# Optimization experiments

Measured on AMD Instinct MI355X. Metric: run time of the kernel, lower is better.

Reference implementation:

```python
import jax, jax.numpy as jnp
import numpy as np

IN_F, OUT_F, RANK = 4096, 4096, 1024
B, S = 4, 2048


def soft_threshold24(w):
    """Soft-threshold 2:4 sparsification along the last dim.
    For each group of 4, the two smallest-magnitude entries are zeroed and the
    kept entries are shrunk by the threshold (2nd-smallest magnitude)."""
    g = w.reshape(-1, 4)
    m = jnp.abs(g)
    t = jnp.sort(m, axis=-1)[:, 1:2]  # largest pruned magnitude per group
    sp = jnp.sign(g) * jnp.maximum(m - t, 0.0)
    return sp.reshape(w.shape)


def fake_fp8_mm(a, b):
    """FP8-simulated GEMM: fp16 operands, fp32 accumulate/output (matches fake_fp8_mm)."""
    return jnp.matmul(a.astype(jnp.float16), b.astype(jnp.float16),
                      preferred_element_type=jnp.float32)


def setup_inputs() -> dict:
    key = jax.random.key(0)
    k1, k2, k3 = jax.random.split(key, 3)
    x = jax.random.normal(k1, (B, S, IN_F), dtype=jnp.float32)
    std_a = (2.0 / (IN_F + RANK)) ** 0.5   # xavier_normal for (in_features, rank)
    std_b = (2.0 / (OUT_F + RANK)) ** 0.5  # xavier_normal for (out_features, rank)
    weight_A = jax.random.normal(k2, (IN_F, RANK), dtype=jnp.float32) * std_a
    weight_B = jax.random.normal(k3, (OUT_F, RANK), dtype=jnp.float32) * std_b
    bias = jnp.zeros((OUT_F,), dtype=jnp.float32)
    scale_A = jnp.ones((), dtype=jnp.float32)  # sparse_init_scale buffer
    scale_B = jnp.ones((), dtype=jnp.float32)
    return {"x": x, "weight_A": weight_A, "weight_B": weight_B, "bias": bias,
            "scale_A": scale_A, "scale_B": scale_B}


def reference(x, weight_A, weight_B, bias, scale_A, scale_B):
    # sparse low-rank factors
    wa = soft_threshold24(weight_A) * scale_A  # (in, rank)
    wb = soft_threshold24(weight_B) * scale_B  # (out, rank)
    lead = x.shape[:-1]
    xf = x.reshape(-1, x.shape[-1])            # (T, in)
    x_proj = fake_fp8_mm(xf, wa)               # (T, rank) == x @ A_sparse
    out = fake_fp8_mm(x_proj, wb.T) + bias     # (T, out) == x_proj @ B_sparse^T + b
    return out.reshape(*lead, OUT_F)
```

## Files before the change

### kernel.cpp

```cpp
#include <hip/hip_runtime.h>

#define IN_FEAT 4096
#define OUT_FEAT 4096
#define RANK 1024
#define TOK 8192

typedef _Float16 f16x8 __attribute__((ext_vector_type(8)));
typedef _Float16 f16x4 __attribute__((ext_vector_type(4)));
typedef float f32x4 __attribute__((ext_vector_type(4)));

#define GLD_LDS16(g, l)                                                         \
  __builtin_amdgcn_global_load_lds(                                             \
      (__attribute__((address_space(1))) const void*)(g),                       \
      (__attribute__((address_space(3))) void*)(l), 16, 0, 0)

#define MIDBAR()                                        \
  __builtin_amdgcn_s_barrier();                         \
  asm volatile("s_waitcnt lgkmcnt(0)" ::: "memory")
#define ENDBAR() __builtin_amdgcn_s_barrier()


__device__ __forceinline__ void soft24(const float4 g, float s,
                                       float& r0, float& r1, float& r2, float& r3) {
  const float m0 = fabsf(g.x), m1 = fabsf(g.y), m2 = fabsf(g.z), m3 = fabsf(g.w);
  const float lo1 = fminf(m0, m1), hi1 = fmaxf(m0, m1);
  const float lo2 = fminf(m2, m3), hi2 = fmaxf(m2, m3);
  const float t = fminf(fmaxf(lo1, lo2), fminf(hi1, hi2));
  r0 = copysignf(fmaxf(m0 - t, 0.0f), g.x) * s;
  r1 = copysignf(fmaxf(m1 - t, 0.0f), g.y) * s;
  r2 = copysignf(fmaxf(m2 - t, 0.0f), g.z) * s;
  r3 = copysignf(fmaxf(m3 - t, 0.0f), g.w) * s;
}

__global__ __launch_bounds__(256) void sparsify_A_kernel(
    const float* __restrict__ wA, const float* __restrict__ scaleA,
    _Float16* __restrict__ waT) {
  const int idx = blockIdx.x * 256 + threadIdx.x;
  const int i = idx & (IN_FEAT - 1);
  const int jg = idx >> 12;
  const float4 g = *reinterpret_cast<const float4*>(wA + (size_t)i * RANK + jg * 4);
  const float s = scaleA[0];
  float r0, r1, r2, r3;
  soft24(g, s, r0, r1, r2, r3);
  const size_t base = (size_t)(jg * 4) * IN_FEAT + i;
  waT[base] = (_Float16)r0;
  waT[base + IN_FEAT] = (_Float16)r1;
  waT[base + 2 * IN_FEAT] = (_Float16)r2;
  waT[base + 3 * IN_FEAT] = (_Float16)r3;
}

__global__ __launch_bounds__(256) void sparsify_B_kernel(
    const float* __restrict__ wB, const float* __restrict__ scaleB,
    _Float16* __restrict__ wbs) {
  const int idx = blockIdx.x * 256 + threadIdx.x;
  const float4 g = *reinterpret_cast<const float4*>(wB + (size_t)idx * 4);
  const float s = scaleB[0];
  float r0, r1, r2, r3;
  soft24(g, s, r0, r1, r2, r3);
  f16x4 h;
  h[0] = (_Float16)r0; h[1] = (_Float16)r1; h[2] = (_Float16)r2; h[3] = (_Float16)r3;
  *reinterpret_cast<f16x4*>(wbs + (size_t)idx * 4) = h;
}

template <int N, int K, bool A_F32, bool OUT_F16>
__global__ __launch_bounds__(256, 4) void gemm128(
    const void* __restrict__ Av, const _Float16* __restrict__ Bh,
    void* __restrict__ Cv, const float* __restrict__ bias) {
  __shared__ __attribute__((aligned(128))) char lds[32768];
  char* ldsA = lds;
  char* ldsB = lds + 16384;

  const int tid = threadIdx.x;
  const int lane = tid & 63;
  const int w = tid >> 6;
  const int wrow = (w >> 1) * 64;
  const int wcol = (w & 1) * 64;

  constexpr int GX = N / 128;
  const int nwg = GX * (TOK / 128);
  const int l = blockIdx.y * GX + blockIdx.x;
  const int wg = (l & 7) * (nwg >> 3) + (l >> 3);
  const int brow = (wg / GX) * 128;
  const int bcol = (wg % GX) * 128;

  f32x4 acc[4][4] = {};

  for (int k0 = 0; k0 < K; k0 += 64) {
    __syncthreads();
#pragma unroll
    for (int it = 0; it < 4; ++it) {
      const int c = it * 256 + tid;
      const int row = c >> 3;
      const int u = c & 7;
      const _Float16* gsrc =
          Bh + (size_t)(bcol + row) * K + k0 + ((u ^ (row & 7)) << 3);
      GLD_LDS16(gsrc, ldsB + c * 16);
    }
    if constexpr (A_F32) {
      const float* Af = (const float*)Av;
#pragma unroll
      for (int it = 0; it < 4; ++it) {
        const int c = it * 256 + tid;
        const int row = c >> 3;
        const int u = c & 7;
        const float* gsrc = Af + (size_t)(brow + row) * K + k0 + (u << 3);
        const float4 f0 = *reinterpret_cast<const float4*>(gsrc);
        const float4 f1 = *reinterpret_cast<const float4*>(gsrc + 4);
        f16x8 h;
        h[0] = (_Float16)f0.x; h[1] = (_Float16)f0.y;
        h[2] = (_Float16)f0.z; h[3] = (_Float16)f0.w;
        h[4] = (_Float16)f1.x; h[5] = (_Float16)f1.y;
        h[6] = (_Float16)f1.z; h[7] = (_Float16)f1.w;
        *reinterpret_cast<f16x8*>(ldsA + row * 128 + ((u ^ (row & 7)) << 4)) = h;
      }
    } else {
      const _Float16* Ah = (const _Float16*)Av;
#pragma unroll
      for (int it = 0; it < 4; ++it) {
        const int c = it * 256 + tid;
        const int row = c >> 3;
        const int u = c & 7;
        const _Float16* gsrc =
            Ah + (size_t)(brow + row) * K + k0 + ((u ^ (row & 7)) << 3);
        GLD_LDS16(gsrc, ldsA + c * 16);
      }
    }
    __syncthreads();
#pragma unroll
    for (int kk = 0; kk < 2; ++kk) {
      f16x8 af[4], bf[4];
#pragma unroll
      for (int m = 0; m < 4; ++m) {
        const int row = wrow + m * 16 + (lane & 15);
        const int u = (kk * 4 + (lane >> 4)) ^ (row & 7);
        af[m] = *reinterpret_cast<const f16x8*>(ldsA + row * 128 + u * 16);
      }
#pragma unroll
      for (int n = 0; n < 4; ++n) {
        const int row = wcol + n * 16 + (lane & 15);
        const int u = (kk * 4 + (lane >> 4)) ^ (row & 7);
        bf[n] = *reinterpret_cast<const f16x8*>(ldsB + row * 128 + u * 16);
      }
#pragma unroll
      for (int m = 0; m < 4; ++m)
#pragma unroll
        for (int n = 0; n < 4; ++n)
          acc[m][n] =
              __builtin_amdgcn_mfma_f32_16x16x32_f16(af[m], bf[n], acc[m][n], 0, 0, 0);
    }
  }

  const int r4 = (lane >> 4) * 4;
  const int cl = lane & 15;
  if constexpr (OUT_F16) {
    _Float16* C = (_Float16*)Cv;
#pragma unroll
    for (int m = 0; m < 4; ++m)
#pragma unroll
      for (int n = 0; n < 4; ++n)
#pragma unroll
        for (int j = 0; j < 4; ++j) {
          const int rr = brow + wrow + m * 16 + r4 + j;
          const int cc = bcol + wcol + n * 16 + cl;
          C[(size_t)rr * N + cc] = (_Float16)acc[m][n][j];
        }
  } else {
    float* C = (float*)Cv;
#pragma unroll
    for (int n = 0; n < 4; ++n) {
      const int cc = bcol + wcol + n * 16 + cl;
      const float bv = bias[cc];
#pragma unroll
      for (int m = 0; m < 4; ++m)
#pragma unroll
        for (int j = 0; j < 4; ++j) {
          const int rr = brow + wrow + m * 16 + r4 + j;
          C[(size_t)rr * N + cc] = acc[m][n][j] + bv;
        }
    }
  }
}

template <int M, int N, int K>
__global__ __launch_bounds__(512, 1) void gemm1_f(
    const float* __restrict__ A, const _Float16* __restrict__ B,
    _Float16* __restrict__ C) {
  extern __shared__ char lds[];

  const int tid = threadIdx.x;
  const int lane = tid & 63;
  const int w = tid >> 6;
  const int wr = w >> 2;
  const int wc = w & 3;
  const int l15 = lane & 15;
  const int ubase = lane >> 4;

  constexpr int GX = N / 256;
  constexpr int NWG = GX * (M / 128);
  const int l = blockIdx.y * GX + blockIdx.x;
  const int wg = (l & 7) * (NWG >> 3) + (l >> 3);
  const int brow = (wg / GX) * 128;
  const int bcol = (wg % GX) * 256;

  f32x4 acc[4][4] = {};
  f16x8 af[4][2], bf[4][2];

  const int ar0 = tid >> 3, au0 = tid & 7;
  const int ar1 = (512 + tid) >> 3, au1 = tid & 7;
  float4 a0l, a0h, a1l, a1h;

  auto issueA = [&](int kof) {
    const float* p0 = A + (size_t)(brow + ar0) * K + kof + au0 * 8;
    const float* p1 = A + (size_t)(brow + ar1) * K + kof + au1 * 8;
    a0l = *reinterpret_cast<const float4*>(p0);
    a0h = *reinterpret_cast<const float4*>(p0 + 4);
    a1l = *reinterpret_cast<const float4*>(p1);
    a1h = *reinterpret_cast<const float4*>(p1 + 4);
  };
  auto writeA = [&](int slot) {
    f16x8 h0, h1;
    h0[0] = (_Float16)a0l.x; h0[1] = (_Float16)a0l.y;
    h0[2] = (_Float16)a0l.z; h0[3] = (_Float16)a0l.w;
    h0[4] = (_Float16)a0h.x; h0[5] = (_Float16)a0h.y;
    h0[6] = (_Float16)a0h.z; h0[7] = (_Float16)a0h.w;
    h1[0] = (_Float16)a1l.x; h1[1] = (_Float16)a1l.y;
    h1[2] = (_Float16)a1l.z; h1[3] = (_Float16)a1l.w;
    h1[4] = (_Float16)a1h.x; h1[5] = (_Float16)a1h.y;
    h1[6] = (_Float16)a1h.z; h1[7] = (_Float16)a1h.w;
    *reinterpret_cast<f16x8*>(lds + slot * 16384 + ar0 * 128 +
                              ((au0 ^ (ar0 & 7)) << 4)) = h0;
    *reinterpret_cast<f16x8*>(lds + slot * 16384 + ar1 * 128 +
                              ((au1 ^ (ar1 & 7)) << 4)) = h1;
  };
  auto stageB = [&](int kof, int slot) {
#pragma unroll
    for (int r = 0; r < 4; ++r) {
      const int c = r * 512 + tid;
      const int row = c >> 3;
      const int u = c & 7;
      GLD_LDS16(B + (size_t)(bcol + row) * K + kof + ((u ^ (row & 7)) << 3),
                lds + 49152 + slot * 32768 + c * 16);
    }
  };

  constexpr int NT = K / 64;

  issueA(0);
  stageB(0, 0);
  asm volatile("s_waitcnt vmcnt(4)" ::: "memory");
  writeA(0);
  issueA(64);
  stageB(64, 1);
  asm volatile("s_waitcnt vmcnt(8)" ::: "memory");
  asm volatile("s_waitcnt lgkmcnt(0)" ::: "memory");
  __builtin_amdgcn_s_barrier();

  int slot = 0;
  for (int t = 0; t < NT; ++t) {
#pragma unroll
    for (int i = 0; i < 4; ++i)
#pragma unroll
      for (int ks = 0; ks < 2; ++ks) {
        const int row = wr * 64 + i * 16 + l15;
        const int u = (ks * 4 + ubase) ^ (row & 7);
        af[i][ks] =
            *reinterpret_cast<const f16x8*>(lds + slot * 16384 + row * 128 + u * 16);
      }
#pragma unroll
    for (int j = 0; j < 4; ++j)
#pragma unroll
      for (int ks = 0; ks < 2; ++ks) {
        const int row = wc * 64 + j * 16 + l15;
        const int u = (ks * 4 + ubase) ^ (row & 7);
        bf[j][ks] = *reinterpret_cast<const f16x8*>(lds + 49152 + slot * 32768 +
                                                    row * 128 + u * 16);
      }
    if (t + 1 < NT) {
      int s1 = slot + 1;
      if (s1 >= 3) s1 -= 3;
      writeA(s1);
    }
    if (t + 2 < NT) {
      int s2 = slot + 2;
      if (s2 >= 3) s2 -= 3;
      issueA((t + 2) * 64);
      stageB((t + 2) * 64, s2);
      asm volatile("s_waitcnt vmcnt(8)" ::: "memory");
    } else {
      asm volatile("s_waitcnt vmcnt(0)" ::: "memory");
    }
    MIDBAR();
    __builtin_amdgcn_s_setprio(1);
#pragma unroll
    for (int ks = 0; ks < 2; ++ks)
#pragma unroll
      for (int i = 0; i < 4; ++i)
#pragma unroll
        for (int j = 0; j < 4; ++j)
          acc[i][j] = __builtin_amdgcn_mfma_f32_16x16x32_f16(
              bf[j][ks], af[i][ks], acc[i][j], 0, 0, 0);
    __builtin_amdgcn_s_setprio(0);
    ENDBAR();
    ++slot;
    if (slot == 3) slot = 0;
  }

  const int r4 = (lane >> 4) * 4;
#pragma unroll
  for (int m = 0; m < 4; ++m)
#pragma unroll
    for (int n = 0; n < 4; ++n) {
      const int rr = brow + wr * 64 + m * 16 + l15;
      const int cc = bcol + wc * 64 + n * 16 + r4;
      f16x4 h;
#pragma unroll
      for (int j = 0; j < 4; ++j) h[j] = (_Float16)acc[m][n][j];
      *reinterpret_cast<f16x4*>(C + (size_t)rr * N + cc) = h;
    }
}

#define AOFF(s, h) (((s) * 2 + (h)) * 16384)
#define BOFF(s, h) (65536 + ((s) * 2 + (h)) * 16384)

template <int M, int N, int K>
__global__ __launch_bounds__(512, 2) void gemm2_m(
    const _Float16* __restrict__ A, const _Float16* __restrict__ B,
    float* __restrict__ C, const float* __restrict__ bias) {
  extern __shared__ char lds[];

  const int tid = threadIdx.x;
  const int lane = tid & 63;
  const int w = tid >> 6;
  const int wr = w >> 2;
  const int wc = w & 3;
  const int l15 = lane & 15;
  const int ubase = lane >> 4;

  constexpr int GX = N / 256;
  constexpr int NWG = GX * (M / 256);
  const int l = blockIdx.y * GX + blockIdx.x;
  const int wg = (l & 7) * (NWG >> 3) + (l >> 3);
  const int brow = (wg / GX) * 256;
  const int bcol = (wg % GX) * 256;

  const _Float16* Abase = A + (size_t)brow * K;
  const _Float16* Bbase = B + (size_t)bcol * K;

  auto stage = [&](const _Float16* srcBase, int rowOff, int kof, int ldsOff) {
#pragma unroll
    for (int r = 0; r < 2; ++r) {
      const int c = r * 512 + tid;
      const int row = c >> 3;
      const int u = c & 7;
      const _Float16* g =
          srcBase + (size_t)(rowOff + row) * K + kof + ((u ^ (row & 7)) << 3);
      GLD_LDS16(g, lds + ldsOff + c * 16);
    }
  };

  f32x4 acc[8][4] = {};
  f16x8 af[4][2], bf01[2][2], bf23[2][2];

#define LDA_GRP(SLOT, MBASE)                                                   \
  _Pragma("unroll") for (int i = 0; i < 4; ++i)                                \
  _Pragma("unroll") for (int ks = 0; ks < 2; ++ks) {                           \
    const int row = ((MBASE) + i) * 16 + l15;                                  \
    const int u = (ks * 4 + ubase) ^ (row & 7);                                \
    af[i][ks] = *reinterpret_cast<const f16x8*>(                               \
        lds + AOFF(SLOT, wr) + row * 128 + u * 16);                            \
  }
#define LDB_GRP(SLOT, NBASE, DST)                                              \
  _Pragma("unroll") for (int j = 0; j < 2; ++j)                                \
  _Pragma("unroll") for (int ks = 0; ks < 2; ++ks) {                           \
    const int row = (wc & 1) * 64 + ((NBASE) + j) * 16 + l15;                  \
    const int u = (ks * 4 + ubase) ^ (row & 7);                                \
    DST[j][ks] = *reinterpret_cast<const f16x8*>(                              \
        lds + BOFF(SLOT, wc >> 1) + row * 128 + u * 16);                       \
  }

#define MFMA32(MO)                                                             \
  __builtin_amdgcn_s_setprio(1);                                               \
  _Pragma("unroll") for (int ks = 0; ks < 2; ++ks)                             \
  _Pragma("unroll") for (int i = 0; i < 4; ++i)                                \
  _Pragma("unroll") for (int j = 0; j < 2; ++j) {                              \
    acc[(MO) + i][j] = __builtin_amdgcn_mfma_f32_16x16x32_f16(                 \
        bf01[j][ks], af[i][ks], acc[(MO) + i][j], 0, 0, 0);                    \
    acc[(MO) + i][2 + j] = __builtin_amdgcn_mfma_f32_16x16x32_f16(             \
        bf23[j][ks], af[i][ks], acc[(MO) + i][2 + j], 0, 0, 0);                \
  }                                                                            \
  __builtin_amdgcn_s_setprio(0);

  constexpr int NT = K / 64;

  stage(Abase, 0, 0, AOFF(0, 0));
  stage(Abase, 128, 0, AOFF(0, 1));
  stage(Bbase, 0, 0, BOFF(0, 0));
  stage(Bbase, 128, 0, BOFF(0, 1));
  stage(Bbase, 0, 64, BOFF(1, 0));
  stage(Bbase, 128, 64, BOFF(1, 1));
  asm volatile("s_waitcnt vmcnt(4)" ::: "memory");
  __builtin_amdgcn_s_barrier();

  for (int tt = 0; tt < NT; tt += 2) {
    const bool last = (tt + 2 >= NT);
    const int kof1 = tt * 64 + 64;
    const int kof2 = tt * 64 + 128;
    const int kof3 = tt * 64 + 192;

    LDA_GRP(0, 0);
    LDB_GRP(0, 0, bf01);
    LDB_GRP(0, 2, bf23);
    stage(Abase, 0, kof1, AOFF(1, 0));
    stage(Abase, 128, kof1, AOFF(1, 1));
    MIDBAR();
    MFMA32(0);
    ENDBAR();

    LDA_GRP(0, 4);
    if (!last) {
      stage(Bbase, 0, kof2, BOFF(0, 0));
      stage(Bbase, 128, kof2, BOFF(0, 1));
      asm volatile("s_waitcnt vmcnt(4)" ::: "memory");
    } else {
      asm volatile("s_waitcnt vmcnt(0)" ::: "memory");
    }
    MIDBAR();
    MFMA32(4);
    ENDBAR();

    LDA_GRP(1, 0);
    LDB_GRP(1, 0, bf01);
    LDB_GRP(1, 2, bf23);
    if (!last) {
      stage(Abase, 0, kof2, AOFF(0, 0));
      stage(Abase, 128, kof2, AOFF(0, 1));
    }
    MIDBAR();
    MFMA32(0);
    ENDBAR();

    LDA_GRP(1, 4);
    if (!last) {
      stage(Bbase, 0, kof3, BOFF(1, 0));
      stage(Bbase, 128, kof3, BOFF(1, 1));
      asm volatile("s_waitcnt vmcnt(4)" ::: "memory");
    }
    MIDBAR();
    MFMA32(4);
    ENDBAR();
  }

  const int r4 = (lane >> 4) * 4;
#pragma unroll
  for (int n = 0; n < 4; ++n) {
    const int cc = bcol + wc * 64 + n * 16 + r4;
    const f32x4 bv = *reinterpret_cast<const f32x4*>(bias + cc);
#pragma unroll
    for (int m = 0; m < 8; ++m) {
      const int rr = brow + wr * 128 + m * 16 + l15;
      f32x4 o = acc[m][n] + bv;
      *reinterpret_cast<f32x4*>(C + (size_t)rr * N + cc) = o;
    }
  }
}


extern "C" void kernel_launch(void* const* d_in, const int* in_sizes, int n_in,
                              void* d_out, int out_size, void* d_ws, size_t ws_size,
                              hipStream_t stream) {
  const float* x = (const float*)d_in[0];
  const float* wA = (const float*)d_in[1];
  const float* wB = (const float*)d_in[2];
  const float* bias = (const float*)d_in[3];
  const float* scaleA = (const float*)d_in[4];
  const float* scaleB = (const float*)d_in[5];
  float* out = (float*)d_out;

  char* ws = (char*)d_ws;
  _Float16* waT = (_Float16*)ws;
  _Float16* wbs = (_Float16*)(ws + (size_t)RANK * IN_FEAT * 2);
  _Float16* xp =
      (_Float16*)(ws + (size_t)RANK * IN_FEAT * 2 + (size_t)OUT_FEAT * RANK * 2);
  const size_t needed = (size_t)RANK * IN_FEAT * 2 + (size_t)OUT_FEAT * RANK * 2 +
                        (size_t)TOK * RANK * 2;

  hipLaunchKernelGGL(sparsify_A_kernel, dim3((IN_FEAT * RANK / 4) / 256), dim3(256),
                     0, stream, wA, scaleA, waT);
  hipLaunchKernelGGL(sparsify_B_kernel, dim3((OUT_FEAT * RANK / 4) / 256), dim3(256),
                     0, stream, wB, scaleB, wbs);

  if (ws_size >= needed) {
    (void)hipFuncSetAttribute(
        reinterpret_cast<const void*>(&gemm1_f<TOK, RANK, IN_FEAT>),
        hipFuncAttributeMaxDynamicSharedMemorySize, 147456);
    hipLaunchKernelGGL((gemm1_f<TOK, RANK, IN_FEAT>),
                       dim3(RANK / 256, TOK / 128), dim3(512), 147456, stream,
                       x, waT, xp);
  } else {
    hipLaunchKernelGGL((gemm128<RANK, IN_FEAT, true, true>),
                       dim3(RANK / 128, TOK / 128), dim3(256), 0, stream,
                       (const void*)x, waT, (void*)xp, nullptr);
  }

  (void)hipFuncSetAttribute(
      reinterpret_cast<const void*>(&gemm2_m<TOK, OUT_FEAT, RANK>),
      hipFuncAttributeMaxDynamicSharedMemorySize, 131072);
  hipLaunchKernelGGL((gemm2_m<TOK, OUT_FEAT, RANK>),
                     dim3(OUT_FEAT / 256, TOK / 256), dim3(512), 131072, stream,
                     xp, wbs, out, bias);
}
```

Measured before the change: 194.7 us.

## Split-K first GEMM into 256x256 tiles with fp32 partials and reduce kernel

Replaces the first GEMM (x @ A_sparse) with a split-K=2 kernel that uses 256x256 output tiles. It converts fp32 x to fp16 in registers before writing it to LDS, and writes fp32 partial sums to workspace. A separate reduce kernel adds the two partials and casts the result to fp16 for the second GEMM. The aim is to raise per-workgroup reuse with larger tiles while keeping enough workgroups (256) to fill the GPU. The cost is 64MB of extra partial-sum traffic, one more kernel launch, and the need for a larger workspace.

New measurement: 222.3 us. +14.2%, slower.

```diff
diff --git a/kernel.cpp b/kernel.cpp
--- a/kernel.cpp
+++ b/kernel.cpp
@@ -60,6 +60,23 @@
   f16x4 h;
   h[0] = (_Float16)r0; h[1] = (_Float16)r1; h[2] = (_Float16)r2; h[3] = (_Float16)r3;
   *reinterpret_cast<f16x4*>(wbs + (size_t)idx * 4) = h;
+}
+
+__global__ __launch_bounds__(256) void reduce_xp_kernel(
+    const float* __restrict__ p0, const float* __restrict__ p1,
+    _Float16* __restrict__ xp) {
+  const size_t i = ((size_t)blockIdx.x * 256 + threadIdx.x) * 8;
+  const f32x4 a0 = *reinterpret_cast<const f32x4*>(p0 + i);
+  const f32x4 a1 = *reinterpret_cast<const f32x4*>(p0 + i + 4);
+  const f32x4 b0 = *reinterpret_cast<const f32x4*>(p1 + i);
+  const f32x4 b1 = *reinterpret_cast<const f32x4*>(p1 + i + 4);
+  const f32x4 s0 = a0 + b0, s1 = a1 + b1;
+  f16x8 h;
+  h[0] = (_Float16)s0[0]; h[1] = (_Float16)s0[1];
+  h[2] = (_Float16)s0[2]; h[3] = (_Float16)s0[3];
+  h[4] = (_Float16)s1[0]; h[5] = (_Float16)s1[1];
+  h[6] = (_Float16)s1[2]; h[7] = (_Float16)s1[3];
+  *reinterpret_cast<f16x8*>(xp + i) = h;
 }
 
 template <int N, int K, bool A_F32, bool OUT_F16>
@@ -322,45 +339,6 @@
 #define AOFF(s, h) (((s) * 2 + (h)) * 16384)
 #define BOFF(s, h) (65536 + ((s) * 2 + (h)) * 16384)
 
-template <int M, int N, int K>
-__global__ __launch_bounds__(512, 2) void gemm2_m(
-    const _Float16* __restrict__ A, const _Float16* __restrict__ B,
-    float* __restrict__ C, const float* __restrict__ bias) {
-  extern __shared__ char lds[];
-
-  const int tid = threadIdx.x;
-  const int lane = tid & 63;
-  const int w = tid >> 6;
-  const int wr = w >> 2;
-  const int wc = w & 3;
-  const int l15 = lane & 15;
-  const int ubase = lane >> 4;
-
-  constexpr int GX = N / 256;
-  constexpr int NWG = GX * (M / 256);
-  const int l = blockIdx.y * GX + blockIdx.x;
-  const int wg = (l & 7) * (NWG >> 3) + (l >> 3);
-  const int brow = (wg / GX) * 256;
-  const int bcol = (wg % GX) * 256;
-
-  const _Float16* Abase = A + (size_t)brow * K;
-  const _Float16* Bbase = B + (size_t)bcol * K;
-
-  auto stage = [&](const _Float16* srcBase, int rowOff, int kof, int ldsOff) {
-#pragma unroll
-    for (int r = 0; r < 2; ++r) {
-      const int c = r * 512 + tid;
-      const int row = c >> 3;
-      const int u = c & 7;
-      const _Float16* g =
-          srcBase + (size_t)(rowOff + row) * K + kof + ((u ^ (row & 7)) << 3);
-      GLD_LDS16(g, lds + ldsOff + c * 16);
-    }
-  };
-
-  f32x4 acc[8][4] = {};
-  f16x8 af[4][2], bf01[2][2], bf23[2][2];
-
 #define LDA_GRP(SLOT, MBASE)                                                   \
   _Pragma("unroll") for (int i = 0; i < 4; ++i)                                \
   _Pragma("unroll") for (int ks = 0; ks < 2; ++ks) {                           \
@@ -377,7 +355,6 @@
     DST[j][ks] = *reinterpret_cast<const f16x8*>(                              \
         lds + BOFF(SLOT, wc >> 1) + row * 128 + u * 16);                       \
   }
-
 #define MFMA32(MO)                                                             \
   __builtin_amdgcn_s_setprio(1);                                               \
   _Pragma("unroll") for (int ks = 0; ks < 2; ++ks)                             \
@@ -390,6 +367,187 @@
   }                                                                            \
   __builtin_amdgcn_s_setprio(0);
 
+template <int M, int N, int LDK, int KSPL>
+__global__ __launch_bounds__(512, 2) void gemm1_sk(
+    const float* __restrict__ A, const _Float16* __restrict__ B,
+    float* __restrict__ P) {
+  extern __shared__ char lds[];
+
+  const int tid = threadIdx.x;
+  const int lane = tid & 63;
+  const int w = tid >> 6;
+  const int wr = w >> 2;
+  const int wc = w & 3;
+  const int l15 = lane & 15;
+  const int ubase = lane >> 4;
+
+  constexpr int GX = N / 256;
+  constexpr int NWG = GX * 2 * (M / 256);
+  const int l = blockIdx.y * (GX * 2) + blockIdx.x;
+  const int wg = (l & 7) * (NWG >> 3) + (l >> 3);
+  const int brow = (wg >> 3) * 256;
+  const int rem = wg & 7;
+  const int bcol = (rem & 3) * 256;
+  const int split = rem >> 2;
+  const int kb = split * (LDK / KSPL);
+
+  const float* Abase = A + (size_t)brow * LDK + kb;
+  const _Float16* Bbase = B + (size_t)bcol * LDK + kb;
+  float* Pout = P + (size_t)split * M * N;
+
+  f32x4 acc[8][4] = {};
+  f16x8 af[4][2], bf01[2][2], bf23[2][2];
+
+  const int sr0 = tid >> 3, su = tid & 7;
+  const int sr1 = (512 + tid) >> 3;
+  float4 g0a, g0b, g1a, g1b;
+
+  auto issueA = [&](int kof, int half) {
+    const float* p0 = Abase + (size_t)(half * 128 + sr0) * LDK + kof + su * 8;
+    const float* p1 = Abase + (size_t)(half * 128 + sr1) * LDK + kof + su * 8;
+    g0a = *reinterpret_cast<const float4*>(p0);
+    g0b = *reinterpret_cast<const float4*>(p0 + 4);
+    g1a = *reinterpret_cast<const float4*>(p1);
+    g1b = *reinterpret_cast<const float4*>(p1 + 4);
+  };
+  auto writeA = [&](int slot, int half) {
+    f16x8 h0, h1;
+    h0[0] = (_Float16)g0a.x; h0[1] = (_Float16)g0a.y;
+    h0[2] = (_Float16)g0a.z; h0[3] = (_Float16)g0a.w;
+    h0[4] = (_Float16)g0b.x; h0[5] = (_Float16)g0b.y;
+    h0[6] = (_Float16)g0b.z; h0[7] = (_Float16)g0b.w;
+    h1[0] = (_Float16)g1a.x; h1[1] = (_Float16)g1a.y;
+    h1[2] = (_Float16)g1a.z; h1[3] = (_Float16)g1a.w;
+    h1[4] = (_Float16)g1b.x; h1[5] = (_Float16)g1b.y;
+    h1[6] = (_Float16)g1b.z; h1[7] = (_Float16)g1b.w;
+    *reinterpret_cast<f16x8*>(lds + AOFF(slot, half) + sr0 * 128 +
+                              ((su ^ (sr0 & 7)) << 4)) = h0;
+    *reinterpret_cast<f16x8*>(lds + AOFF(slot, half) + sr1 * 128 +
+                              ((su ^ (sr1 & 7)) << 4)) = h1;
+  };
+  auto stageB = [&](int kof, int slot) {
+#pragma unroll
+    for (int h = 0; h < 2; ++h)
+#pragma unroll
+      for (int r = 0; r < 2; ++r) {
+        const int c = r * 512 + tid;
+        const int row = c >> 3, u = c & 7;
+        GLD_LDS16(Bbase + (size_t)(h * 128 + row) * LDK + kof + ((u ^ (row & 7)) << 3),
+                  lds + BOFF(slot, h) + c * 16);
+      }
+  };
+
+  constexpr int NT = (LDK / KSPL) / 64;
+
+  issueA(0, 0);
+  stageB(0, 0);
+  writeA(0, 0);
+  issueA(0, 1);
+  writeA(0, 1);
+  issueA(64, 0);
+  stageB(64, 1);
+  asm volatile("s_waitcnt vmcnt(8)" ::: "memory");
+  asm volatile("s_waitcnt lgkmcnt(0)" ::: "memory");
+  __builtin_amdgcn_s_barrier();
+
+  for (int tt = 0; tt < NT; tt += 2) {
+    const bool pre = (tt + 2 < NT);
+    const int kof1 = tt * 64 + 64;
+    const int kof2 = tt * 64 + 128;
+    const int kof3 = tt * 64 + 192;
+
+    LDA_GRP(0, 0);
+    LDB_GRP(0, 0, bf01);
+    LDB_GRP(0, 2, bf23);
+    writeA(1, 0);
+    issueA(kof1, 1);
+    MIDBAR();
+    MFMA32(0);
+    ENDBAR();
+
+    LDA_GRP(0, 4);
+    writeA(1, 1);
+    if (pre) {
+      issueA(kof2, 0);
+      stageB(kof2, 0);
+    }
+    MIDBAR();
+    MFMA32(4);
+    ENDBAR();
+
+    LDA_GRP(1, 0);
+    LDB_GRP(1, 0, bf01);
+    LDB_GRP(1, 2, bf23);
+    if (pre) {
+      writeA(0, 0);
+      issueA(kof2, 1);
+    }
+    MIDBAR();
+    MFMA32(0);
+    ENDBAR();
+
+    LDA_GRP(1, 4);
+    if (pre) {
+      writeA(0, 1);
+      issueA(kof3, 0);
+      stageB(kof3, 1);
+    }
+    MIDBAR();
+    MFMA32(4);
+    ENDBAR();
+  }
+
+  const int r4 = (lane >> 4) * 4;
+#pragma unroll
+  for (int n = 0; n < 4; ++n) {
+    const int cc = bcol + wc * 64 + n * 16 + r4;
+#pragma unroll
+    for (int m = 0; m < 8; ++m) {
+      const int rr = brow + wr * 128 + m * 16 + l15;
+      *reinterpret_cast<f32x4*>(Pout + (size_t)rr * N + cc) = acc[m][n];
+    }
+  }
+}
+
+template <int M, int N, int K>
+__global__ __launch_bounds__(512, 2) void gemm2_m(
+    const _Float16* __restrict__ A, const _Float16* __restrict__ B,
+    float* __restrict__ C, const float* __restrict__ bias) {
+  extern __shared__ char lds[];
+
+  const int tid = threadIdx.x;
+  const int lane = tid & 63;
+  const int w = tid >> 6;
+  const int wr = w >> 2;
+  const int wc = w & 3;
+  const int l15 = lane & 15;
+  const int ubase = lane >> 4;
+
+  constexpr int GX = N / 256;
+  constexpr int NWG = GX * (M / 256);
+  const int l = blockIdx.y * GX + blockIdx.x;
+  const int wg = (l & 7) * (NWG >> 3) + (l >> 3);
+  const int brow = (wg / GX) * 256;
+  const int bcol = (wg % GX) * 256;
+
+  const _Float16* Abase = A + (size_t)brow * K;
+  const _Float16* Bbase = B + (size_t)bcol * K;
+
+  auto stage = [&](const _Float16* srcBase, int rowOff, int kof, int ldsOff) {
+#pragma unroll
+    for (int r = 0; r < 2; ++r) {
+      const int c = r * 512 + tid;
+      const int row = c >> 3;
+      const int u = c & 7;
+      const _Float16* g =
+          srcBase + (size_t)(rowOff + row) * K + kof + ((u ^ (row & 7)) << 3);
+      GLD_LDS16(g, lds + ldsOff + c * 16);
+    }
+  };
+
+  f32x4 acc[8][4] = {};
+  f16x8 af[4][2], bf01[2][2], bf23[2][2];
+
   constexpr int NT = K / 64;
 
   stage(Abase, 0, 0, AOFF(0, 0));
@@ -481,15 +639,27 @@
   _Float16* wbs = (_Float16*)(ws + (size_t)RANK * IN_FEAT * 2);
   _Float16* xp =
       (_Float16*)(ws + (size_t)RANK * IN_FEAT * 2 + (size_t)OUT_FEAT * RANK * 2);
-  const size_t needed = (size_t)RANK * IN_FEAT * 2 + (size_t)OUT_FEAT * RANK * 2 +
-                        (size_t)TOK * RANK * 2;
+  float* part = (float*)(ws + (size_t)RANK * IN_FEAT * 2 +
+                         (size_t)OUT_FEAT * RANK * 2 + (size_t)TOK * RANK * 2);
+  const size_t needed_f = (size_t)RANK * IN_FEAT * 2 + (size_t)OUT_FEAT * RANK * 2 +
+                          (size_t)TOK * RANK * 2;
+  const size_t needed_sk = needed_f + (size_t)2 * TOK * RANK * 4;
 
   hipLaunchKernelGGL(sparsify_A_kernel, dim3((IN_FEAT * RANK / 4) / 256), dim3(256),
                      0, stream, wA, scaleA, waT);
   hipLaunchKernelGGL(sparsify_B_kernel, dim3((OUT_FEAT * RANK / 4) / 256), dim3(256),
                      0, stream, wB, scaleB, wbs);
 
-  if (ws_size >= needed) {
+  if (ws_size >= needed_sk) {
+    (void)hipFuncSetAttribute(
+        reinterpret_cast<const void*>(&gemm1_sk<TOK, RANK, IN_FEAT, 2>),
+        hipFuncAttributeMaxDynamicSharedMemorySize, 131072);
+    hipLaunchKernelGGL((gemm1_sk<TOK, RANK, IN_FEAT, 2>),
+                       dim3(RANK / 256 * 2, TOK / 256), dim3(512), 131072, stream,
+                       x, waT, part);
+    hipLaunchKernelGGL(reduce_xp_kernel, dim3((TOK * RANK / 8) / 256), dim3(256),
+                       0, stream, part, part + (size_t)TOK * RANK, xp);
+  } else if (ws_size >= needed_f) {
     (void)hipFuncSetAttribute(
         reinterpret_cast<const void*>(&gemm1_f<TOK, RANK, IN_FEAT>),
         hipFuncAttributeMaxDynamicSharedMemorySize, 147456);
```
